# Optimization experiments

Hardware: AMD Instinct MI355X
Metric: run time of the kernel (lower is better)

Reference implementation:

```python
import jax, jax.numpy as jnp
import numpy as np

LOG2PI = float(np.log(2.0 * np.pi))

N, M, K = 16384, 4096, 64


def setup_inputs() -> dict:
    key = jax.random.key(0)
    ks = jax.random.split(key, 6)
    x = jax.random.normal(ks[0], (N, M), dtype=jnp.float32)
    noise = jax.random.normal(ks[1], (N, K), dtype=jnp.float32)
    # small init scale so linear outputs stay numerically tame
    W_enc_mu = jax.random.normal(ks[2], (M, K), dtype=jnp.float32) * 0.02
    b_enc_mu = jnp.zeros((K,), dtype=jnp.float32)
    W_enc_sigma = jax.random.normal(ks[3], (M, 1), dtype=jnp.float32) * 0.002
    b_enc_sigma = jnp.ones((1,), dtype=jnp.float32)
    W_dec_mu = jax.random.normal(ks[4], (K, M), dtype=jnp.float32) * 0.02
    b_dec_mu = jnp.zeros((M,), dtype=jnp.float32)
    W_dec_sigma = jax.random.normal(ks[5], (K, 1), dtype=jnp.float32) * 0.002
    b_dec_sigma = jnp.ones((1,), dtype=jnp.float32)
    return dict(x=x, noise=noise, W_enc_mu=W_enc_mu, b_enc_mu=b_enc_mu,
                W_enc_sigma=W_enc_sigma, b_enc_sigma=b_enc_sigma,
                W_dec_mu=W_dec_mu, b_dec_mu=b_dec_mu,
                W_dec_sigma=W_dec_sigma, b_dec_sigma=b_dec_sigma)


def _iso_mvn_logpdf(x, mu, var, d):
    # log N(x; mu, var * I_d), var: [n] per-sample scalar variance
    sq = jnp.sum((x - mu) ** 2, axis=-1)  # [n]
    return -0.5 * (d * LOG2PI + d * jnp.log(var) + sq / var)


def reference(x, noise, W_enc_mu, b_enc_mu, W_enc_sigma, b_enc_sigma,
              W_dec_mu, b_dec_mu, W_dec_sigma, b_dec_sigma):
    n, m = x.shape
    k = W_enc_mu.shape[1]
    # encoder
    z_mu = x @ W_enc_mu + b_enc_mu              # [n, k]
    s_enc = x @ W_enc_sigma + b_enc_sigma       # [n, 1]
    # reparametrize: z = mu + sigma^2 * noise (as in original)
    z = z_mu + (s_enc ** 2) * noise             # [n, k]
    # decoder
    x_mu = z @ W_dec_mu + b_dec_mu              # [n, m]
    s_dec = z @ W_dec_sigma + b_dec_sigma       # [n, 1]
    # original squares sigma then squares again inside _expand_batch_sigma:
    # diagonal covariance value = sigma^4
    var_z = (s_enc[:, 0] ** 4)                  # [n]
    var_x = (s_dec[:, 0] ** 4)                  # [n]
    log_posterior = _iso_mvn_logpdf(z, z_mu, var_z, k)          # [n]
    log_likelihood = _iso_mvn_logpdf(x, x_mu, var_x, m)         # [n]
    log_prior = -0.5 * (k * LOG2PI + jnp.sum(z ** 2, axis=-1))  # [n]
    lb = jnp.sum(log_posterior - log_likelihood - log_prior)
    return lb.reshape(1)
```

## Files before the change

### kernel.cpp

```cpp
#include <hip/hip_runtime.h>
#include <hip/hip_bf16.h>

#define LOG2PI 1.8378770664093453f


typedef __attribute__((ext_vector_type(8))) short bf16x8;
typedef __attribute__((ext_vector_type(4))) float f32x4;

__device__ __forceinline__ unsigned short f2bf(float f) {
    unsigned int u = __builtin_bit_cast(unsigned int, f);
    u += 0x7FFFu + ((u >> 16) & 1u);
    return (unsigned short)(u >> 16);
}
__device__ __forceinline__ short f2bf_s(float f) {
    return (short)__builtin_bit_cast(unsigned short, __float2bfloat16(f));
}
__device__ __forceinline__ void gll16(const void* g, void* l) {
    __builtin_amdgcn_global_load_lds(
        (const __attribute__((address_space(1))) void*)g,
        (__attribute__((address_space(3))) void*)l, 16, 0, 0);
}

__global__ __launch_bounds__(256) void pack_b_kernel(const float* __restrict__ We,
        const float* __restrict__ Wes, const float* __restrict__ Wd,
        const float* __restrict__ bd, unsigned char* __restrict__ Bp) {
    __shared__ float WeL[2048];
    __shared__ float WdL[2048];
    __shared__ float WesL[32], bdL[32];
    const int kt = blockIdx.x;
    const int t = threadIdx.x;
#pragma unroll
    for (int i = 0; i < 2; ++i) {
        int q = t + 256 * i;
        *reinterpret_cast<f32x4*>(WeL + q * 4) =
            *reinterpret_cast<const f32x4*>(We + (size_t)kt * 2048 + q * 4);
    }
#pragma unroll
    for (int i = 0; i < 2; ++i) {
        int f = t + 256 * i;
        int r = f >> 3, s4 = f & 7;
        *reinterpret_cast<f32x4*>(WdL + r * 32 + s4 * 4) =
            *reinterpret_cast<const f32x4*>(Wd + (size_t)r * 4096 + kt * 32 + s4 * 4);
    }
    if (t < 8) {
        *reinterpret_cast<f32x4*>(WesL + t * 4) =
            *reinterpret_cast<const f32x4*>(Wes + kt * 32 + t * 4);
    } else if (t < 16) {
        int q = t - 8;
        *reinterpret_cast<f32x4*>(bdL + q * 4) =
            *reinterpret_cast<const f32x4*>(bd + kt * 32 + q * 4);
    }
    __syncthreads();
#pragma unroll
    for (int i = 0; i < 3; ++i) {
        int cidx = t + 256 * i;
        int col = cidx >> 2, u = cidx & 3;
        int ku = u ^ (col & 3);
        unsigned short out[8];
#pragma unroll
        for (int j = 0; j < 8; ++j) {
            int ml = ku * 8 + j;
            float v = 0.f;
            if (col < 64)        v = WeL[ml * 64 + col];
            else if (col < 128)  v = WdL[(col - 64) * 32 + ml];
            else if (col == 128) v = WesL[ml];
            else if (col == 129) v = bdL[ml];
            out[j] = f2bf(v);
        }
        *reinterpret_cast<uint4*>(Bp + ((size_t)kt * 768 + cidx) * 16) =
            *reinterpret_cast<uint4*>(out);
    }
}

__global__ __launch_bounds__(256) void prep_g_kernel(const float* __restrict__ Wd,
        const float* __restrict__ bd, float* __restrict__ G,
        float* __restrict__ hv, float* __restrict__ ev) {
    __shared__ float red[256];
    const int b = blockIdx.x, t = threadIdx.x;
    float p = 0.f;
    if (b < 4096) {
        int a = b >> 6, c = b & 63;
        const f32x4* ra = reinterpret_cast<const f32x4*>(Wd + (size_t)a * 4096);
        const f32x4* rc = reinterpret_cast<const f32x4*>(Wd + (size_t)c * 4096);
        for (int j = t; j < 1024; j += 256) {
            f32x4 u = ra[j], v = rc[j];
            p += u[0] * v[0] + u[1] * v[1] + u[2] * v[2] + u[3] * v[3];
        }
    } else if (b < 4160) {
        int a = b - 4096;
        const f32x4* ra = reinterpret_cast<const f32x4*>(Wd + (size_t)a * 4096);
        const f32x4* rb = reinterpret_cast<const f32x4*>(bd);
        for (int j = t; j < 1024; j += 256) {
            f32x4 u = ra[j], v = rb[j];
            p += u[0] * v[0] + u[1] * v[1] + u[2] * v[2] + u[3] * v[3];
        }
    } else {
        const f32x4* rb = reinterpret_cast<const f32x4*>(bd);
        for (int j = t; j < 1024; j += 256) {
            f32x4 v = rb[j];
            p += v[0] * v[0] + v[1] * v[1] + v[2] * v[2] + v[3] * v[3];
        }
    }
    red[t] = p;
    __syncthreads();
    for (int s = 128; s > 0; s >>= 1) { if (t < s) red[t] += red[t + s]; __syncthreads(); }
    if (t == 0) {
        if (b < 4096) G[b] = red[0];
        else if (b < 4160) hv[b - 4096] = red[0];
        else ev[0] = red[0];
    }
}

__global__ __launch_bounds__(256, 4) void gemm_kernel(const float* __restrict__ x,
        const unsigned char* __restrict__ Bp, float* __restrict__ Pp,
        int steps, int kslice, int ppstride) {
    __shared__ __align__(16) char lds[40960];
    char* ldsA = lds;
    char* ldsB = lds + 16384;
    const int tid = threadIdx.x;
    const int lane = tid & 63, w = tid >> 6;
    const int wm = w >> 1, wn = w & 1;
    const int l15 = lane & 15, kg = lane >> 4;
    const int rowbase = blockIdx.x * 64;
    const int ks = blockIdx.y;

    const float* xA[2];
    {
        int rsub = lane >> 3;
        int co = ((lane & 7) ^ rsub) << 2;
#pragma unroll
        for (int i = 0; i < 2; ++i)
            xA[i] = x + (size_t)(rowbase + (w * 2 + i) * 8 + rsub) * 4096
                      + (size_t)ks * kslice + co;
    }
    const unsigned char* gB0 = Bp + (size_t)(ks * steps) * 12288
                                  + (size_t)(w * 3) * 1024 + (size_t)lane * 16;

    f32x4 acc[2][5];
#pragma unroll
    for (int mi = 0; mi < 2; ++mi)
#pragma unroll
        for (int ni = 0; ni < 5; ++ni) acc[mi][ni] = (f32x4){0.f, 0.f, 0.f, 0.f};
    float sxa0 = 0.f, sxa1 = 0.f;

#define STAGE(buf, tt) do { \
        _Pragma("unroll") \
        for (int i_ = 0; i_ < 2; ++i_) \
            gll16(xA[i_] + (tt) * 32, ldsA + (buf) * 8192 + (w * 2 + i_) * 1024); \
        _Pragma("unroll") \
        for (int j_ = 0; j_ < 3; ++j_) \
            gll16(gB0 + (size_t)(tt) * 12288 + j_ * 1024, \
                  ldsB + (buf) * 12288 + (w * 3 + j_) * 1024); \
    } while (0)

#define COMPUTE(buf) do { \
        char* A0 = ldsA + (buf) * 8192; \
        char* B0 = ldsB + (buf) * 12288; \
        bf16x8 bfr[5]; \
        _Pragma("unroll") \
        for (int ni_ = 0; ni_ < 5; ++ni_) { \
            int col_ = wn * 80 + ni_ * 16 + l15; \
            bfr[ni_] = *reinterpret_cast<const bf16x8*>( \
                B0 + col_ * 64 + ((kg ^ (col_ & 3)) << 4)); \
        } \
        _Pragma("unroll") \
        for (int mi_ = 0; mi_ < 2; ++mi_) { \
            int row_ = wm * 32 + mi_ * 16 + l15; \
            int e0_ = (kg << 1) ^ (row_ & 7); \
            f32x4 fa_ = *reinterpret_cast<const f32x4*>(A0 + row_ * 128 + (e0_ << 4)); \
            f32x4 fb_ = *reinterpret_cast<const f32x4*>(A0 + row_ * 128 + ((e0_ ^ 1) << 4)); \
            bf16x8 af_; \
            af_[0] = f2bf_s(fa_[0]); af_[1] = f2bf_s(fa_[1]); \
            af_[2] = f2bf_s(fa_[2]); af_[3] = f2bf_s(fa_[3]); \
            af_[4] = f2bf_s(fb_[0]); af_[5] = f2bf_s(fb_[1]); \
            af_[6] = f2bf_s(fb_[2]); af_[7] = f2bf_s(fb_[3]); \
            if (wn == 0) { \
                float ss_ = fa_[0]*fa_[0] + fa_[1]*fa_[1] + fa_[2]*fa_[2] + fa_[3]*fa_[3] \
                          + fb_[0]*fb_[0] + fb_[1]*fb_[1] + fb_[2]*fb_[2] + fb_[3]*fb_[3]; \
                if (mi_ == 0) sxa0 += ss_; else sxa1 += ss_; \
            } \
            _Pragma("unroll") \
            for (int ni_ = 0; ni_ < 5; ++ni_) \
                acc[mi_][ni_] = __builtin_amdgcn_mfma_f32_16x16x32_bf16( \
                    af_, bfr[ni_], acc[mi_][ni_], 0, 0, 0); \
        } \
    } while (0)

    STAGE(0, 0);
    asm volatile("s_waitcnt vmcnt(0)" ::: "memory");
    __builtin_amdgcn_s_barrier();
    asm volatile("" ::: "memory");
    int cur = 0;
    for (int t = 0; t < steps - 1; ++t) {
        STAGE(cur ^ 1, t + 1);
        asm volatile("s_waitcnt vmcnt(5)" ::: "memory");
        __builtin_amdgcn_s_barrier();
        asm volatile("" ::: "memory");
        COMPUTE(cur);
        asm volatile("" ::: "memory");
        __builtin_amdgcn_s_barrier();
        cur ^= 1;
    }
    asm volatile("s_waitcnt vmcnt(0)" ::: "memory");
    __builtin_amdgcn_s_barrier();
    asm volatile("" ::: "memory");
    COMPUTE(cur);
#undef STAGE
#undef COMPUTE

    sxa0 += __shfl_xor(sxa0, 16); sxa0 += __shfl_xor(sxa0, 32);
    sxa1 += __shfl_xor(sxa1, 16); sxa1 += __shfl_xor(sxa1, 32);

    __syncthreads();
    float* C = reinterpret_cast<float*>(lds);
#pragma unroll
    for (int mi = 0; mi < 2; ++mi)
#pragma unroll
        for (int ni = 0; ni < 5; ++ni) {
            int col = wn * 80 + ni * 16 + l15;
            if (col < 148 && col != 130) {
#pragma unroll
                for (int i2 = 0; i2 < 4; ++i2)
                    C[(wm * 32 + mi * 16 + kg * 4 + i2) * 148 + col] = acc[mi][ni][i2];
            }
        }
    if (wn == 0 && lane < 16) {
        C[(wm * 32 + lane) * 148 + 130] = sxa0;
        C[(wm * 32 + 16 + lane) * 148 + 130] = sxa1;
    }
    __syncthreads();
#pragma unroll
    for (int i = 0; i < 9; ++i) {
        int idx = tid + 256 * i;
        int r = idx / 36, c4 = idx % 36;
        f32x4 v = *reinterpret_cast<const f32x4*>(C + r * 148 + c4 * 4);
        *reinterpret_cast<f32x4*>(Pp + (size_t)(rowbase + r) * ppstride + ks * 144 + c4 * 4) = v;
    }
}

__global__ __launch_bounds__(256) void phase2_kernel(const float* __restrict__ Pp,
        const float* __restrict__ noise, const float* __restrict__ bem,
        const float* __restrict__ Wds, const float* __restrict__ bes_p,
        const float* __restrict__ bds_p, const float* __restrict__ G,
        const float* __restrict__ hv, const float* __restrict__ ev,
        float* __restrict__ partial, int ksplit, int ppstride) {
    __shared__ float Gl[4096];
    __shared__ float hl[64], wl[64], beml[64];
    __shared__ float zs[4][64];
    __shared__ float red[4];
    int tid = threadIdx.x;
    for (int i = tid; i < 4096; i += 256) Gl[i] = G[i];
    if (tid < 64) { hl[tid] = hv[tid]; wl[tid] = Wds[tid]; beml[tid] = bem[tid]; }
    __syncthreads();
    float bes = bes_p[0], bds = bds_p[0], e = ev[0];
    int wid = tid >> 6, k = tid & 63;
    const int sw = (k & 15) << 2;
    float wacc = 0.f;
#pragma unroll
    for (int rr = 0; rr < 8; ++rr) {
        int row = blockIdx.x * 32 + wid * 8 + rr;
        const float* base = Pp + (size_t)row * ppstride;
        float zmu = beml[k], ck = 0.f, se = bes, dd = 0.f, sx2 = 0.f;
        for (int s = 0; s < ksplit; ++s) {
            const float* b2 = base + s * 144;
            zmu += b2[k]; ck += b2[64 + k];
            se += b2[128]; dd += b2[129]; sx2 += b2[130];
        }
        float nz = noise[(size_t)row * 64 + k];
        float s2 = se * se;
        float z = fmaf(s2, nz, zmu);
        zs[wid][k] = z;
        float t0 = 0.f, t1 = 0.f, t2 = 0.f, t3 = 0.f;
        const float* gr = &Gl[k * 64];
        const float* zr = &zs[wid][0];
#pragma unroll
        for (int jb = 0; jb < 16; ++jb) {
            int p = (jb * 4) ^ sw;
            f32x4 gv = *reinterpret_cast<const f32x4*>(gr + p);
            f32x4 zv = *reinterpret_cast<const f32x4*>(zr + p);
            t0 = fmaf(gv[0], zv[0], t0); t1 = fmaf(gv[1], zv[1], t1);
            t2 = fmaf(gv[2], zv[2], t2); t3 = fmaf(gv[3], zv[3], t3);
        }
        float t = (t0 + t1) + (t2 + t3);
        float ra = z * z;
        float rb = nz * nz;
        float rc = z * wl[k];
        float rd = z * ck;
        float re = z * fmaf(2.f, hl[k], t);
#pragma unroll
        for (int d = 1; d < 64; d <<= 1) {
            ra += __shfl_xor(ra, d); rb += __shfl_xor(rb, d);
            rc += __shfl_xor(rc, d); rd += __shfl_xor(rd, d);
            re += __shfl_xor(re, d);
        }
        float sdec = rc + bds;
        float xxmu = rd + dd;
        float xmu2 = re + e;
        float sq_lik = sx2 - 2.f * xxmu + xmu2;
        float vz = s2 * s2;
        float sd2 = sdec * sdec;
        float vx = sd2 * sd2;
        wacc += 0.5f * (4096.f * LOG2PI + 4096.f * __logf(vx) + sq_lik / vx
                        + ra - 64.f * __logf(vz) - rb);
    }
    if (k == 0) red[wid] = wacc;
    __syncthreads();
    if (tid == 0) partial[blockIdx.x] = red[0] + red[1] + red[2] + red[3];
}

__global__ __launch_bounds__(256) void final_reduce_kernel(const float* __restrict__ partial,
                                                           float* __restrict__ out) {
    __shared__ float red[4];
    int tid = threadIdx.x;
    float v = 0.f;
    for (int i = tid; i < 512; i += 256) v += partial[i];
#pragma unroll
    for (int d = 1; d < 64; d <<= 1) v += __shfl_xor(v, d);
    if ((tid & 63) == 0) red[tid >> 6] = v;
    __syncthreads();
    if (tid == 0) out[0] = red[0] + red[1] + red[2] + red[3];
}

extern "C" void kernel_launch(void* const* d_in, const int* in_sizes, int n_in,
                              void* d_out, int out_size, void* d_ws, size_t ws_size,
                              hipStream_t stream) {
    const float* x     = (const float*)d_in[0];
    const float* noise = (const float*)d_in[1];
    const float* We    = (const float*)d_in[2];
    const float* bem   = (const float*)d_in[3];
    const float* Wes   = (const float*)d_in[4];
    const float* bes   = (const float*)d_in[5];
    const float* Wd    = (const float*)d_in[6];
    const float* bdm   = (const float*)d_in[7];
    const float* Wds   = (const float*)d_in[8];
    const float* bds   = (const float*)d_in[9];

    int ksplit = (ws_size >= 39340544ull) ? 4 : (ws_size >= 20466176ull ? 2 : 1);
    int steps = 128 / ksplit;
    int kslice = steps * 32;
    int ppstride = ksplit * 144;

    char* ws = (char*)d_ws;
    size_t ppbytes = (size_t)16384 * ppstride * 4;
    float* Pp           = (float*)ws;
    unsigned char* Bp   = (unsigned char*)(ws + ppbytes);
    float* G            = (float*)(ws + ppbytes + 1572864);
    float* hv           = (float*)(ws + ppbytes + 1572864 + 16384);
    float* ev           = (float*)(ws + ppbytes + 1572864 + 16640);
    float* partial      = (float*)(ws + ppbytes + 1572864 + 16896);

    pack_b_kernel<<<128, 256, 0, stream>>>(We, Wes, Wd, bdm, Bp);
    prep_g_kernel<<<4161, 256, 0, stream>>>(Wd, bdm, G, hv, ev);
    gemm_kernel<<<dim3(256, ksplit), 256, 0, stream>>>(x, Bp, Pp, steps, kslice, ppstride);
    phase2_kernel<<<512, 256, 0, stream>>>(Pp, noise, bem, Wds, bes, bds, G, hv, ev,
                                           partial, ksplit, ppstride);
    final_reduce_kernel<<<1, 256, 0, stream>>>(partial, (float*)d_out);
}
```

Baseline: 122.5 us.

## Double GEMM K-tile to 64 and overlap next-tile prefetch with compute

The GEMM K-step grows from 32 to 64, with the packed B layout, LDS swizzles and staging addresses reworked to match. This halves the number of pipeline iterations and barriers. The loop now issues the next stage's loads before computing the current buffer, then waits once per iteration instead of twice. LDS use rises to 72KB, so occupancy bounds drop from 4 to 2 blocks per CU, which may reduce latency hiding.

```diff
diff --git a/kernel.cpp b/kernel.cpp
--- a/kernel.cpp
+++ b/kernel.cpp
@@ -24,50 +24,50 @@
 __global__ __launch_bounds__(256) void pack_b_kernel(const float* __restrict__ We,
         const float* __restrict__ Wes, const float* __restrict__ Wd,
         const float* __restrict__ bd, unsigned char* __restrict__ Bp) {
-    __shared__ float WeL[2048];
-    __shared__ float WdL[2048];
-    __shared__ float WesL[32], bdL[32];
+    __shared__ float WeL[4096];
+    __shared__ float WdL[4096];
+    __shared__ float WesL[64], bdL[64];
     const int kt = blockIdx.x;
     const int t = threadIdx.x;
 #pragma unroll
-    for (int i = 0; i < 2; ++i) {
+    for (int i = 0; i < 4; ++i) {
         int q = t + 256 * i;
         *reinterpret_cast<f32x4*>(WeL + q * 4) =
-            *reinterpret_cast<const f32x4*>(We + (size_t)kt * 2048 + q * 4);
-    }
-#pragma unroll
-    for (int i = 0; i < 2; ++i) {
+            *reinterpret_cast<const f32x4*>(We + (size_t)kt * 4096 + q * 4);
+    }
+#pragma unroll
+    for (int i = 0; i < 4; ++i) {
         int f = t + 256 * i;
-        int r = f >> 3, s4 = f & 7;
-        *reinterpret_cast<f32x4*>(WdL + r * 32 + s4 * 4) =
-            *reinterpret_cast<const f32x4*>(Wd + (size_t)r * 4096 + kt * 32 + s4 * 4);
-    }
-    if (t < 8) {
+        int r = f >> 4, s4 = f & 15;
+        *reinterpret_cast<f32x4*>(WdL + r * 64 + s4 * 4) =
+            *reinterpret_cast<const f32x4*>(Wd + (size_t)r * 4096 + kt * 64 + s4 * 4);
+    }
+    if (t < 16) {
         *reinterpret_cast<f32x4*>(WesL + t * 4) =
-            *reinterpret_cast<const f32x4*>(Wes + kt * 32 + t * 4);
-    } else if (t < 16) {
-        int q = t - 8;
+            *reinterpret_cast<const f32x4*>(Wes + kt * 64 + t * 4);
+    } else if (t < 32) {
+        int q = t - 16;
         *reinterpret_cast<f32x4*>(bdL + q * 4) =
-            *reinterpret_cast<const f32x4*>(bd + kt * 32 + q * 4);
-    }
-    __syncthreads();
-#pragma unroll
-    for (int i = 0; i < 3; ++i) {
+            *reinterpret_cast<const f32x4*>(bd + kt * 64 + q * 4);
+    }
+    __syncthreads();
+#pragma unroll
+    for (int i = 0; i < 5; ++i) {
         int cidx = t + 256 * i;
-        int col = cidx >> 2, u = cidx & 3;
-        int ku = u ^ (col & 3);
+        int col = cidx >> 3, u = cidx & 7;
+        int ku = u ^ (col & 7);
         unsigned short out[8];
 #pragma unroll
         for (int j = 0; j < 8; ++j) {
-            int ml = ku * 8 + j;
+            int m = ku * 8 + j;
             float v = 0.f;
-            if (col < 64)        v = WeL[ml * 64 + col];
-            else if (col < 128)  v = WdL[(col - 64) * 32 + ml];
-            else if (col == 128) v = WesL[ml];
-            else if (col == 129) v = bdL[ml];
+            if (col < 64)        v = WeL[m * 64 + col];
+            else if (col < 128)  v = WdL[(col - 64) * 64 + m];
+            else if (col == 128) v = WesL[m];
+            else if (col == 129) v = bdL[m];
             out[j] = f2bf(v);
         }
-        *reinterpret_cast<uint4*>(Bp + ((size_t)kt * 768 + cidx) * 16) =
+        *reinterpret_cast<uint4*>(Bp + ((size_t)kt * 1280 + cidx) * 16) =
             *reinterpret_cast<uint4*>(out);
     }
 }
@@ -111,12 +111,10 @@
     }
 }
 
-__global__ __launch_bounds__(256, 4) void gemm_kernel(const float* __restrict__ x,
+__global__ __launch_bounds__(256, 2) void gemm_kernel(const float* __restrict__ x,
         const unsigned char* __restrict__ Bp, float* __restrict__ Pp,
         int steps, int kslice, int ppstride) {
-    __shared__ __align__(16) char lds[40960];
-    char* ldsA = lds;
-    char* ldsB = lds + 16384;
+    __shared__ __align__(16) char lds[73728];
     const int tid = threadIdx.x;
     const int lane = tid & 63, w = tid >> 6;
     const int wm = w >> 1, wn = w & 1;
@@ -124,17 +122,16 @@
     const int rowbase = blockIdx.x * 64;
     const int ks = blockIdx.y;
 
-    const float* xA[2];
-    {
-        int rsub = lane >> 3;
-        int co = ((lane & 7) ^ rsub) << 2;
-#pragma unroll
-        for (int i = 0; i < 2; ++i)
-            xA[i] = x + (size_t)(rowbase + (w * 2 + i) * 8 + rsub) * 4096
-                      + (size_t)ks * kslice + co;
-    }
-    const unsigned char* gB0 = Bp + (size_t)(ks * steps) * 12288
-                                  + (size_t)(w * 3) * 1024 + (size_t)lane * 16;
+    const float* xA[4];
+#pragma unroll
+    for (int i = 0; i < 4; ++i) {
+        int rloc = w * 16 + i * 4 + (lane >> 4);
+        int co = ((lane & 15) ^ (rloc & 15)) << 2;
+        xA[i] = x + (size_t)(rowbase + rloc) * 4096 + (size_t)ks * kslice + co;
+    }
+    const unsigned char* gB0 = Bp + (size_t)(w * 5) * 1024 + (size_t)lane * 16;
+    const int ldsAoff = (w * 16) * 256 + lane * 16;
+    const int ldsBoff = (w * 5) * 1024 + lane * 16;
 
     f32x4 acc[2][5];
 #pragma unroll
@@ -145,44 +142,49 @@
 
 #define STAGE(buf, tt) do { \
         _Pragma("unroll") \
-        for (int i_ = 0; i_ < 2; ++i_) \
-            gll16(xA[i_] + (tt) * 32, ldsA + (buf) * 8192 + (w * 2 + i_) * 1024); \
+        for (int i_ = 0; i_ < 4; ++i_) \
+            gll16(xA[i_] + (tt) * 64, lds + (buf) * 36864 + ldsAoff + i_ * 1024); \
         _Pragma("unroll") \
-        for (int j_ = 0; j_ < 3; ++j_) \
-            gll16(gB0 + (size_t)(tt) * 12288 + j_ * 1024, \
-                  ldsB + (buf) * 12288 + (w * 3 + j_) * 1024); \
+        for (int j_ = 0; j_ < 5; ++j_) \
+            gll16(gB0 + (size_t)(ks * steps + (tt)) * 20480 + j_ * 1024, \
+                  lds + (buf) * 36864 + 16384 + ldsBoff + j_ * 1024); \
     } while (0)
 
 #define COMPUTE(buf) do { \
-        char* A0 = ldsA + (buf) * 8192; \
-        char* B0 = ldsB + (buf) * 12288; \
-        bf16x8 bfr[5]; \
+        char* A0 = lds + (buf) * 36864; \
+        char* B0 = A0 + 16384; \
         _Pragma("unroll") \
-        for (int ni_ = 0; ni_ < 5; ++ni_) { \
-            int col_ = wn * 80 + ni_ * 16 + l15; \
-            bfr[ni_] = *reinterpret_cast<const bf16x8*>( \
-                B0 + col_ * 64 + ((kg ^ (col_ & 3)) << 4)); \
-        } \
-        _Pragma("unroll") \
-        for (int mi_ = 0; mi_ < 2; ++mi_) { \
-            int row_ = wm * 32 + mi_ * 16 + l15; \
-            int e0_ = (kg << 1) ^ (row_ & 7); \
-            f32x4 fa_ = *reinterpret_cast<const f32x4*>(A0 + row_ * 128 + (e0_ << 4)); \
-            f32x4 fb_ = *reinterpret_cast<const f32x4*>(A0 + row_ * 128 + ((e0_ ^ 1) << 4)); \
-            bf16x8 af_; \
-            af_[0] = f2bf_s(fa_[0]); af_[1] = f2bf_s(fa_[1]); \
-            af_[2] = f2bf_s(fa_[2]); af_[3] = f2bf_s(fa_[3]); \
-            af_[4] = f2bf_s(fb_[0]); af_[5] = f2bf_s(fb_[1]); \
-            af_[6] = f2bf_s(fb_[2]); af_[7] = f2bf_s(fb_[3]); \
-            if (wn == 0) { \
-                float ss_ = fa_[0]*fa_[0] + fa_[1]*fa_[1] + fa_[2]*fa_[2] + fa_[3]*fa_[3] \
-                          + fb_[0]*fb_[0] + fb_[1]*fb_[1] + fb_[2]*fb_[2] + fb_[3]*fb_[3]; \
-                if (mi_ == 0) sxa0 += ss_; else sxa1 += ss_; \
+        for (int kk_ = 0; kk_ < 2; ++kk_) { \
+            bf16x8 bfr[5]; \
+            _Pragma("unroll") \
+            for (int ni_ = 0; ni_ < 5; ++ni_) { \
+                int col_ = wn * 80 + ni_ * 16 + l15; \
+                bfr[ni_] = *reinterpret_cast<const bf16x8*>( \
+                    B0 + col_ * 128 + (((kk_ * 4 + kg) ^ (col_ & 7)) << 4)); \
             } \
             _Pragma("unroll") \
-            for (int ni_ = 0; ni_ < 5; ++ni_) \
-                acc[mi_][ni_] = __builtin_amdgcn_mfma_f32_16x16x32_bf16( \
-                    af_, bfr[ni_], acc[mi_][ni_], 0, 0, 0); \
+            for (int mi_ = 0; mi_ < 2; ++mi_) { \
+                int row_ = wm * 32 + mi_ * 16 + l15; \
+                int u0_ = kk_ * 8 + kg * 2; \
+                f32x4 fa_ = *reinterpret_cast<const f32x4*>( \
+                    A0 + row_ * 256 + (((u0_) ^ (row_ & 15)) << 4)); \
+                f32x4 fb_ = *reinterpret_cast<const f32x4*>( \
+                    A0 + row_ * 256 + (((u0_ + 1) ^ (row_ & 15)) << 4)); \
+                bf16x8 af_; \
+                af_[0] = f2bf_s(fa_[0]); af_[1] = f2bf_s(fa_[1]); \
+                af_[2] = f2bf_s(fa_[2]); af_[3] = f2bf_s(fa_[3]); \
+                af_[4] = f2bf_s(fb_[0]); af_[5] = f2bf_s(fb_[1]); \
+                af_[6] = f2bf_s(fb_[2]); af_[7] = f2bf_s(fb_[3]); \
+                if (wn == 0) { \
+                    float ss_ = fa_[0]*fa_[0] + fa_[1]*fa_[1] + fa_[2]*fa_[2] + fa_[3]*fa_[3] \
+                              + fb_[0]*fb_[0] + fb_[1]*fb_[1] + fb_[2]*fb_[2] + fb_[3]*fb_[3]; \
+                    if (mi_ == 0) sxa0 += ss_; else sxa1 += ss_; \
+                } \
+                _Pragma("unroll") \
+                for (int ni_ = 0; ni_ < 5; ++ni_) \
+                    acc[mi_][ni_] = __builtin_amdgcn_mfma_f32_16x16x32_bf16( \
+                        af_, bfr[ni_], acc[mi_][ni_], 0, 0, 0); \
+            } \
         } \
     } while (0)
 
@@ -191,20 +193,14 @@
     __builtin_amdgcn_s_barrier();
     asm volatile("" ::: "memory");
     int cur = 0;
-    for (int t = 0; t < steps - 1; ++t) {
-        STAGE(cur ^ 1, t + 1);
-        asm volatile("s_waitcnt vmcnt(5)" ::: "memory");
+    for (int t = 0; t < steps; ++t) {
+        if (t + 1 < steps) STAGE(cur ^ 1, t + 1);
+        COMPUTE(cur);
+        asm volatile("s_waitcnt vmcnt(0)" ::: "memory");
         __builtin_amdgcn_s_barrier();
         asm volatile("" ::: "memory");
-        COMPUTE(cur);
-        asm volatile("" ::: "memory");
-        __builtin_amdgcn_s_barrier();
         cur ^= 1;
     }
-    asm volatile("s_waitcnt vmcnt(0)" ::: "memory");
-    __builtin_amdgcn_s_barrier();
-    asm volatile("" ::: "memory");
-    COMPUTE(cur);
 #undef STAGE
 #undef COMPUTE
 
@@ -336,8 +332,8 @@
     const float* bds   = (const float*)d_in[9];
 
     int ksplit = (ws_size >= 39340544ull) ? 4 : (ws_size >= 20466176ull ? 2 : 1);
-    int steps = 128 / ksplit;
-    int kslice = steps * 32;
+    int steps = 64 / ksplit;
+    int kslice = steps * 64;
     int ppstride = ksplit * 144;
 
     char* ws = (char*)d_ws;
@@ -349,7 +345,7 @@
     float* ev           = (float*)(ws + ppbytes + 1572864 + 16640);
     float* partial      = (float*)(ws + ppbytes + 1572864 + 16896);
 
-    pack_b_kernel<<<128, 256, 0, stream>>>(We, Wes, Wd, bdm, Bp);
+    pack_b_kernel<<<64, 256, 0, stream>>>(We, Wes, Wd, bdm, Bp);
     prep_g_kernel<<<4161, 256, 0, stream>>>(Wd, bdm, G, hv, ev);
     gemm_kernel<<<dim3(256, ksplit), 256, 0, stream>>>(x, Bp, Pp, steps, kslice, ppstride);
     phase2_kernel<<<512, 256, 0, stream>>>(Pp, noise, bem, Wds, bes, bds, G, hv, ev,
```

Result: slower. 131.4 us (+7.3%).

## Double GEMM row tile to 128 rows per block and reswizzle B layout

Applied to the files above, without the earlier changes.

The GEMM block now covers 128 rows instead of 64, with each warp owning 64 rows (4 MFMA row tiles). This halves how often the packed B panel is reloaded per row of x and raises the number of MFMAs per B fragment load. The B pack swizzle changes to (col + col>>2)&3 to reduce LDS bank conflicts. The epilogue is staged in two passes through LDS. The cost is more LDS (56 KB) and more registers, so occupancy drops to 2 blocks per CU and the grid is half as large.

```diff
diff --git a/kernel.cpp b/kernel.cpp
--- a/kernel.cpp
+++ b/kernel.cpp
@@ -55,7 +55,7 @@
     for (int i = 0; i < 3; ++i) {
         int cidx = t + 256 * i;
         int col = cidx >> 2, u = cidx & 3;
-        int ku = u ^ (col & 3);
+        int ku = u ^ ((col + (col >> 2)) & 3);
         unsigned short out[8];
 #pragma unroll
         for (int j = 0; j < 8; ++j) {
@@ -111,61 +111,58 @@
     }
 }
 
-__global__ __launch_bounds__(256, 4) void gemm_kernel(const float* __restrict__ x,
+__global__ __launch_bounds__(256, 2) void gemm_kernel(const float* __restrict__ x,
         const unsigned char* __restrict__ Bp, float* __restrict__ Pp,
         int steps, int kslice, int ppstride) {
-    __shared__ __align__(16) char lds[40960];
-    char* ldsA = lds;
-    char* ldsB = lds + 16384;
+    __shared__ __align__(16) char lds[57344];
     const int tid = threadIdx.x;
     const int lane = tid & 63, w = tid >> 6;
     const int wm = w >> 1, wn = w & 1;
     const int l15 = lane & 15, kg = lane >> 4;
-    const int rowbase = blockIdx.x * 64;
+    const int rowbase = blockIdx.x * 128;
     const int ks = blockIdx.y;
 
-    const float* xA[2];
-    {
-        int rsub = lane >> 3;
-        int co = ((lane & 7) ^ rsub) << 2;
-#pragma unroll
-        for (int i = 0; i < 2; ++i)
-            xA[i] = x + (size_t)(rowbase + (w * 2 + i) * 8 + rsub) * 4096
-                      + (size_t)ks * kslice + co;
-    }
-    const unsigned char* gB0 = Bp + (size_t)(ks * steps) * 12288
-                                  + (size_t)(w * 3) * 1024 + (size_t)lane * 16;
-
-    f32x4 acc[2][5];
-#pragma unroll
-    for (int mi = 0; mi < 2; ++mi)
+    const float* xA[4];
+#pragma unroll
+    for (int i = 0; i < 4; ++i) {
+        int q = i * 256 + tid;
+        int row = q >> 3, u8 = q & 7;
+        int co = (u8 ^ (row & 7)) << 2;
+        xA[i] = x + (size_t)(rowbase + row) * 4096 + (size_t)ks * kslice + co;
+    }
+    const unsigned char* gB0 = Bp + (size_t)tid * 16;
+
+    f32x4 acc[4][5];
+#pragma unroll
+    for (int mi = 0; mi < 4; ++mi)
 #pragma unroll
         for (int ni = 0; ni < 5; ++ni) acc[mi][ni] = (f32x4){0.f, 0.f, 0.f, 0.f};
-    float sxa0 = 0.f, sxa1 = 0.f;
+    float sxa[4] = {0.f, 0.f, 0.f, 0.f};
 
 #define STAGE(buf, tt) do { \
         _Pragma("unroll") \
-        for (int i_ = 0; i_ < 2; ++i_) \
-            gll16(xA[i_] + (tt) * 32, ldsA + (buf) * 8192 + (w * 2 + i_) * 1024); \
+        for (int i_ = 0; i_ < 4; ++i_) \
+            gll16(xA[i_] + (tt) * 32, lds + (buf) * 28672 + i_ * 4096 + tid * 16); \
         _Pragma("unroll") \
         for (int j_ = 0; j_ < 3; ++j_) \
-            gll16(gB0 + (size_t)(tt) * 12288 + j_ * 1024, \
-                  ldsB + (buf) * 12288 + (w * 3 + j_) * 1024); \
+            gll16(gB0 + (size_t)(ks * steps + (tt)) * 12288 + j_ * 4096, \
+                  lds + (buf) * 28672 + 16384 + j_ * 4096 + tid * 16); \
     } while (0)
 
 #define COMPUTE(buf) do { \
-        char* A0 = ldsA + (buf) * 8192; \
-        char* B0 = ldsB + (buf) * 12288; \
+        char* A0 = lds + (buf) * 28672; \
+        char* B0 = A0 + 16384; \
         bf16x8 bfr[5]; \
         _Pragma("unroll") \
         for (int ni_ = 0; ni_ < 5; ++ni_) { \
             int col_ = wn * 80 + ni_ * 16 + l15; \
+            int q_ = (col_ + (col_ >> 2)) & 3; \
             bfr[ni_] = *reinterpret_cast<const bf16x8*>( \
-                B0 + col_ * 64 + ((kg ^ (col_ & 3)) << 4)); \
+                B0 + col_ * 64 + ((kg ^ q_) << 4)); \
         } \
         _Pragma("unroll") \
-        for (int mi_ = 0; mi_ < 2; ++mi_) { \
-            int row_ = wm * 32 + mi_ * 16 + l15; \
+        for (int mi_ = 0; mi_ < 4; ++mi_) { \
+            int row_ = wm * 64 + mi_ * 16 + l15; \
             int e0_ = (kg << 1) ^ (row_ & 7); \
             f32x4 fa_ = *reinterpret_cast<const f32x4*>(A0 + row_ * 128 + (e0_ << 4)); \
             f32x4 fb_ = *reinterpret_cast<const f32x4*>(A0 + row_ * 128 + ((e0_ ^ 1) << 4)); \
@@ -175,9 +172,8 @@
             af_[4] = f2bf_s(fb_[0]); af_[5] = f2bf_s(fb_[1]); \
             af_[6] = f2bf_s(fb_[2]); af_[7] = f2bf_s(fb_[3]); \
             if (wn == 0) { \
-                float ss_ = fa_[0]*fa_[0] + fa_[1]*fa_[1] + fa_[2]*fa_[2] + fa_[3]*fa_[3] \
+                sxa[mi_] += fa_[0]*fa_[0] + fa_[1]*fa_[1] + fa_[2]*fa_[2] + fa_[3]*fa_[3] \
                           + fb_[0]*fb_[0] + fb_[1]*fb_[1] + fb_[2]*fb_[2] + fb_[3]*fb_[3]; \
-                if (mi_ == 0) sxa0 += ss_; else sxa1 += ss_; \
             } \
             _Pragma("unroll") \
             for (int ni_ = 0; ni_ < 5; ++ni_) \
@@ -193,7 +189,7 @@
     int cur = 0;
     for (int t = 0; t < steps - 1; ++t) {
         STAGE(cur ^ 1, t + 1);
-        asm volatile("s_waitcnt vmcnt(5)" ::: "memory");
+        asm volatile("s_waitcnt vmcnt(7)" ::: "memory");
         __builtin_amdgcn_s_barrier();
         asm volatile("" ::: "memory");
         COMPUTE(cur);
@@ -208,33 +204,43 @@
 #undef STAGE
 #undef COMPUTE
 
-    sxa0 += __shfl_xor(sxa0, 16); sxa0 += __shfl_xor(sxa0, 32);
-    sxa1 += __shfl_xor(sxa1, 16); sxa1 += __shfl_xor(sxa1, 32);
-
-    __syncthreads();
+#pragma unroll
+    for (int mi = 0; mi < 4; ++mi) {
+        sxa[mi] += __shfl_xor(sxa[mi], 16);
+        sxa[mi] += __shfl_xor(sxa[mi], 32);
+    }
+
     float* C = reinterpret_cast<float*>(lds);
 #pragma unroll
-    for (int mi = 0; mi < 2; ++mi)
-#pragma unroll
-        for (int ni = 0; ni < 5; ++ni) {
-            int col = wn * 80 + ni * 16 + l15;
-            if (col < 148 && col != 130) {
-#pragma unroll
-                for (int i2 = 0; i2 < 4; ++i2)
-                    C[(wm * 32 + mi * 16 + kg * 4 + i2) * 148 + col] = acc[mi][ni][i2];
+    for (int pass = 0; pass < 2; ++pass) {
+        __syncthreads();
+        if (wm == pass) {
+#pragma unroll
+            for (int mi = 0; mi < 4; ++mi)
+#pragma unroll
+                for (int ni = 0; ni < 5; ++ni) {
+                    int col = wn * 80 + ni * 16 + l15;
+                    if (col < 148 && col != 130) {
+#pragma unroll
+                        for (int i2 = 0; i2 < 4; ++i2)
+                            C[(mi * 16 + kg * 4 + i2) * 148 + col] = acc[mi][ni][i2];
+                    }
+                }
+            if (wn == 0 && lane < 16) {
+#pragma unroll
+                for (int mi = 0; mi < 4; ++mi)
+                    C[(mi * 16 + lane) * 148 + 130] = sxa[mi];
             }
         }
-    if (wn == 0 && lane < 16) {
-        C[(wm * 32 + lane) * 148 + 130] = sxa0;
-        C[(wm * 32 + 16 + lane) * 148 + 130] = sxa1;
-    }
-    __syncthreads();
-#pragma unroll
-    for (int i = 0; i < 9; ++i) {
-        int idx = tid + 256 * i;
-        int r = idx / 36, c4 = idx % 36;
-        f32x4 v = *reinterpret_cast<const f32x4*>(C + r * 148 + c4 * 4);
-        *reinterpret_cast<f32x4*>(Pp + (size_t)(rowbase + r) * ppstride + ks * 144 + c4 * 4) = v;
+        __syncthreads();
+#pragma unroll
+        for (int i = 0; i < 9; ++i) {
+            int idx = tid + 256 * i;
+            int r = idx / 36, c4 = idx % 36;
+            f32x4 v = *reinterpret_cast<const f32x4*>(C + r * 148 + c4 * 4);
+            *reinterpret_cast<f32x4*>(
+                Pp + (size_t)(rowbase + pass * 64 + r) * ppstride + ks * 144 + c4 * 4) = v;
+        }
     }
 }
 
@@ -351,7 +357,7 @@
 
     pack_b_kernel<<<128, 256, 0, stream>>>(We, Wes, Wd, bdm, Bp);
     prep_g_kernel<<<4161, 256, 0, stream>>>(Wd, bdm, G, hv, ev);
-    gemm_kernel<<<dim3(256, ksplit), 256, 0, stream>>>(x, Bp, Pp, steps, kslice, ppstride);
+    gemm_kernel<<<dim3(128, ksplit), 256, 0, stream>>>(x, Bp, Pp, steps, kslice, ppstride);
     phase2_kernel<<<512, 256, 0, stream>>>(Pp, noise, bem, Wds, bes, bds, G, hv, ev,
                                            partial, ksplit, ppstride);
     final_reduce_kernel<<<1, 256, 0, stream>>>(partial, (float*)d_out);
```

After: 116.6 us. 1.05x faster.
